# Optimization experiments

Measured on AMD Instinct MI355X. Metric: run time of the kernel, lower is better.

## Reference

```python
import jax, jax.numpy as jnp
import numpy as np


def reference(x, y, max_disp):
    # x, y: [B, C, H, W] left/right feature maps (stride-3 features)
    # Builds cost[b, :C, i, h, w]  = x[b, :, h, w]      for w >= i else 0
    #        cost[b, C:, i, h, w] = y[b, :, h, w - i]  for w >= i else 0
    # i.e. the vectorized form of the original Python loop over disparities.
    D = max_disp // 3
    B, C, H, W = x.shape
    d = jnp.arange(D)
    w = jnp.arange(W)
    mask = (w[None, :] >= d[:, None]).astype(x.dtype)          # [D, W]
    m = mask[None, None, :, None, :]                            # [1,1,D,1,W]
    cost_x = x[:, :, None, :, :] * m                            # [B,C,D,H,W]
    idx = jnp.clip(w[None, :] - d[:, None], 0, W - 1)           # [D, W]
    y_shift = y[:, :, :, idx]                                   # [B,C,H,D,W]
    cost_y = jnp.transpose(y_shift, (0, 1, 3, 2, 4)) * m        # [B,C,D,H,W]
    return jnp.concatenate([cost_x, cost_y], axis=1)            # [B,2C,D,H,W]


def setup_inputs() -> dict:
    key = jax.random.key(0)
    k1, k2 = jax.random.split(key)
    B, C, H, W = 1, 32, 96, 192
    x = jax.random.normal(k1, (B, C, H, W), dtype=jnp.float32)
    y = jax.random.normal(k2, (B, C, H, W), dtype=jnp.float32)
    return {"x": x, "y": y, "max_disp": 192}
```

## Files before the change

### kernel.cpp

```cpp
#include <hip/hip_runtime.h>

constexpr int C  = 32;
constexpr int D  = 64;
constexpr int H  = 96;
constexpr int W  = 192;
constexpr int W4 = W / 4;

__global__ __launch_bounds__(256) void fusion_kernel(const float* __restrict__ x,
                                                     const float* __restrict__ y,
                                                     float4* __restrict__ out) {
    const int tid = blockIdx.x * blockDim.x + threadIdx.x;
    const int w4   = tid % W4;
    int rest       = tid / W4;
    const int h    = rest % H;
    rest          /= H;
    const int d    = rest % D;
    const int ch   = rest / D;
    const int w    = w4 * 4;

    float4 v;
    if (ch < C) {
        v = *(const float4*)(&x[(ch * H + h) * W + w]);
    } else {
        const float* yr = &y[((ch - C) * H + h) * W];
        v.x = yr[max(w + 0 - d, 0)];
        v.y = yr[max(w + 1 - d, 0)];
        v.z = yr[max(w + 2 - d, 0)];
        v.w = yr[max(w + 3 - d, 0)];
    }
    if (w < d) {
        if (w + 0 < d) v.x = 0.f;
        if (w + 1 < d) v.y = 0.f;
        if (w + 2 < d) v.z = 0.f;
        if (w + 3 < d) v.w = 0.f;
    }
    out[tid] = v;
}

extern "C" void kernel_launch(void* const* d_in, const int* in_sizes, int n_in,
                              void* d_out, int out_size, void* d_ws, size_t ws_size,
                              hipStream_t stream) {
    const float* x = (const float*)d_in[0];
    const float* y = (const float*)d_in[1];
    float4* out    = (float4*)d_out;

    constexpr int total4 = 2 * C * D * H * W4;
    constexpr int block  = 256;
    constexpr int grid   = total4 / block;
    fusion_kernel<<<grid, block, 0, stream>>>(x, y, out);
}
```

Before: 350.0 us.

## Process disparity chunks per thread with sliding y window and nontemporal stores

Each thread now produces 16 consecutive disparity slices for one channel/row/w4 position instead of one. The x row is loaded once and reused, and y values are shifted through registers with one new load per disparity. Output writes use nontemporal stores to avoid polluting cache with the large write-only output. Fewer threads do more work each, which could reduce parallelism or latency hiding.

```diff
diff --git a/kernel.cpp b/kernel.cpp
--- a/kernel.cpp
+++ b/kernel.cpp
@@ -1,40 +1,65 @@
 #include <hip/hip_runtime.h>
 
-constexpr int C  = 32;
-constexpr int D  = 64;
-constexpr int H  = 96;
-constexpr int W  = 192;
-constexpr int W4 = W / 4;
+constexpr int C      = 32;
+constexpr int D      = 64;
+constexpr int H      = 96;
+constexpr int W      = 192;
+constexpr int W4     = W / 4;
+constexpr int DCHUNK = 16;
+constexpr int NCHUNK = D / DCHUNK;
+
+typedef float f4 __attribute__((ext_vector_type(4)));
 
 __global__ __launch_bounds__(256) void fusion_kernel(const float* __restrict__ x,
                                                      const float* __restrict__ y,
-                                                     float4* __restrict__ out) {
-    const int tid = blockIdx.x * blockDim.x + threadIdx.x;
+                                                     float* __restrict__ out) {
+    const int tid  = blockIdx.x * blockDim.x + threadIdx.x;
     const int w4   = tid % W4;
     int rest       = tid / W4;
     const int h    = rest % H;
     rest          /= H;
-    const int d    = rest % D;
-    const int ch   = rest / D;
+    const int ch   = rest % (2 * C);
+    const int d0   = (rest / (2 * C)) * DCHUNK;
     const int w    = w4 * 4;
 
-    float4 v;
+    int outoff = (ch * D + d0) * (H * W) + h * W + w;
+
     if (ch < C) {
-        v = *(const float4*)(&x[(ch * H + h) * W + w]);
+        const f4 xv = *(const f4*)(&x[(ch * H + h) * W + w]);
+        #pragma unroll
+        for (int i = 0; i < DCHUNK; ++i) {
+            const int d = d0 + i;
+            f4 v = xv;
+            if (w < d) {
+                if (w + 0 < d) v.x = 0.f;
+                if (w + 1 < d) v.y = 0.f;
+                if (w + 2 < d) v.z = 0.f;
+                if (w + 3 < d) v.w = 0.f;
+            }
+            __builtin_nontemporal_store(v, (f4*)(&out[outoff + i * (H * W)]));
+        }
     } else {
         const float* yr = &y[((ch - C) * H + h) * W];
-        v.x = yr[max(w + 0 - d, 0)];
-        v.y = yr[max(w + 1 - d, 0)];
-        v.z = yr[max(w + 2 - d, 0)];
-        v.w = yr[max(w + 3 - d, 0)];
+        f4 v;
+        v.x = yr[max(w + 0 - d0, 0)];
+        v.y = yr[max(w + 1 - d0, 0)];
+        v.z = yr[max(w + 2 - d0, 0)];
+        v.w = yr[max(w + 3 - d0, 0)];
+        #pragma unroll
+        for (int i = 0; i < DCHUNK; ++i) {
+            const int d = d0 + i;
+            f4 s = v;
+            if (w < d) {
+                if (w + 0 < d) s.x = 0.f;
+                if (w + 1 < d) s.y = 0.f;
+                if (w + 2 < d) s.z = 0.f;
+                if (w + 3 < d) s.w = 0.f;
+            }
+            __builtin_nontemporal_store(s, (f4*)(&out[outoff + i * (H * W)]));
+            v.w = v.z; v.z = v.y; v.y = v.x;
+            v.x = yr[max(w - d - 1, 0)];
+        }
     }
-    if (w < d) {
-        if (w + 0 < d) v.x = 0.f;
-        if (w + 1 < d) v.y = 0.f;
-        if (w + 2 < d) v.z = 0.f;
-        if (w + 3 < d) v.w = 0.f;
-    }
-    out[tid] = v;
 }
 
 extern "C" void kernel_launch(void* const* d_in, const int* in_sizes, int n_in,
@@ -42,10 +67,10 @@
                               hipStream_t stream) {
     const float* x = (const float*)d_in[0];
     const float* y = (const float*)d_in[1];
-    float4* out    = (float4*)d_out;
+    float* out     = (float*)d_out;
 
-    constexpr int total4 = 2 * C * D * H * W4;
+    constexpr int total  = 2 * C * H * W4 * NCHUNK;
     constexpr int block  = 256;
-    constexpr int grid   = total4 / block;
+    constexpr int grid   = total / block;
     fusion_kernel<<<grid, block, 0, stream>>>(x, y, out);
 }
```

New measurement: 305.1 us. 1.15x faster.
